# Performance work log

Measured on AMD Instinct MI355X. Metric: run time of the kernel, lower is better.

The kernel has to match this reference:

```python
import jax, jax.numpy as jnp
import numpy as np

IN_C, OUT_C, MAX_SIZE = 512, 256, 256
N = MAX_SIZE * MAX_SIZE  # 65536 nodes
E = MAX_SIZE * MAX_SIZE  # 65536 edges (before self loops)
NEG_SLOPE = 0.2


def setup_inputs() -> dict:
    key = jax.random.key(0)
    ks = jax.random.split(key, 12)
    s = 1.0 / np.sqrt(IN_C)
    so = 1.0 / np.sqrt(OUT_C)
    return {
        "x": jax.random.normal(ks[0], (N, IN_C), dtype=jnp.float32),
        "x_mask": jnp.ones((N,), dtype=bool),
        "edge_index": jax.random.randint(ks[1], (2, E), 0, N),
        "edge_mask": jnp.ones((E,), dtype=bool),
        "vaild_mask": jnp.ones((MAX_SIZE, MAX_SIZE), dtype=bool),
        # self-loop Linear
        "W_self": jax.random.uniform(ks[2], (IN_C, OUT_C), jnp.float32, -s, s),
        "b_self": jax.random.uniform(ks[3], (OUT_C,), jnp.float32, -s, s),
        # GATv2Conv params (heads=1)
        "W_l": jax.random.uniform(ks[4], (IN_C, OUT_C), jnp.float32, -s, s),
        "b_l": jnp.zeros((OUT_C,), jnp.float32),
        "W_r": jax.random.uniform(ks[5], (IN_C, OUT_C), jnp.float32, -s, s),
        "b_r": jnp.zeros((OUT_C,), jnp.float32),
        "att": jax.random.uniform(ks[6], (OUT_C,), jnp.float32, -so, so),
        "conv_bias": jnp.zeros((OUT_C,), jnp.float32),
        # sk classifier (out_channels -> 1)
        "W_cls": jax.random.uniform(ks[7], (OUT_C, 1), jnp.float32, -so, so),
        "b_cls": jax.random.uniform(ks[8], (1,), jnp.float32, -so, so),
    }


def _forward(x, edge_index, W_self, b_self, W_l, b_l, W_r, b_r, att,
             conv_bias, W_cls, b_cls):
    n = x.shape[0]
    # PyG GATv2Conv adds self-loops by default
    loops = jnp.arange(n, dtype=edge_index.dtype)
    src = jnp.concatenate([edge_index[0], loops])
    dst = jnp.concatenate([edge_index[1], loops])

    x_l = x @ W_l + b_l  # source-side transform (n, out)
    x_r = x @ W_r + b_r  # target-side transform (n, out)

    # per-edge GATv2 attention logits
    h = jax.nn.leaky_relu(x_l[src] + x_r[dst], NEG_SLOPE)  # (Etot, out)
    e = h @ att  # (Etot,)

    # segment softmax over incoming edges of each target node
    m = jnp.full((n,), -jnp.inf, dtype=e.dtype).at[dst].max(e)
    p = jnp.exp(e - m[dst])
    denom = jax.ops.segment_sum(p, dst, num_segments=n)
    alpha = p / denom[dst]

    x_neigh = jax.ops.segment_sum(alpha[:, None] * x_l[src], dst,
                                  num_segments=n) + conv_bias
    x_out = (x @ W_self + b_self) + x_neigh

    # sinkhorn-style row softmax channel (sk_channel=1, n1=n2=max_size)
    ms = MAX_SIZE
    sk = (x_out @ W_cls + b_cls).reshape(ms, ms)
    sk = jax.nn.softmax(sk, axis=-1)
    x_out = x_out + sk.reshape(-1, 1)
    # n1*n2 == max_size**2, so the padded output equals x_out
    return x_out


def reference(x, x_mask, edge_index, edge_mask, vaild_mask, W_self, b_self,
              W_l, b_l, W_r, b_r, att, conv_bias, W_cls, b_cls):
    # masks are all-True (fully valid case): x_valid = x, edges all kept
    return _forward(x, edge_index, W_self, b_self, W_l, b_l, W_r, b_r, att,
                    conv_bias, W_cls, b_cls)
```

## Files before the change

kernel.cpp:

```cpp
#include <hip/hip_runtime.h>
#include <hip/hip_bf16.h>
#include <stdint.h>

#define NNODE 65536
#define NEDGE 65536
#define ETOT  (NNODE + NEDGE)
#define INC   512
#define OUTC  256
#define NEG_SLOPE 0.2f
#define SLOTCAP 32

typedef __attribute__((ext_vector_type(8))) __bf16 bf16x8;
typedef __attribute__((ext_vector_type(4))) float f32x4;

__device__ __forceinline__ float b2f(unsigned short u) {
  return __uint_as_float(((unsigned int)u) << 16);
}
__device__ __forceinline__ unsigned short f2b(float f) {
  unsigned int u = __float_as_uint(f);
  u += 0x7fffu + ((u >> 16) & 1u);
  return (unsigned short)(u >> 16);
}
__device__ __forceinline__ unsigned int pk2(float lo, float hi) {
  return (unsigned int)f2b(lo) | ((unsigned int)f2b(hi) << 16);
}
__device__ __forceinline__ float lrelu(float v) {
  return v > 0.f ? v : NEG_SLOPE * v;
}

__global__ __launch_bounds__(256) void cvt_x_kernel(const float* __restrict__ x,
                                                    unsigned short* __restrict__ xb) {
  size_t i = ((size_t)blockIdx.x * 256 + threadIdx.x) * 4;
  float4 v = *(const float4*)(x + i);
  ushort4 o = { f2b(v.x), f2b(v.y), f2b(v.z), f2b(v.w) };
  *(ushort4*)(xb + i) = o;
}

__global__ __launch_bounds__(256) void prep_w_kernel(
    const float* __restrict__ Wl, const float* __restrict__ Wr, const float* __restrict__ Ws,
    const float* __restrict__ bl, const float* __restrict__ br, const float* __restrict__ bs,
    unsigned short* __restrict__ WT, float* __restrict__ bcat) {
  int i = blockIdx.x * 256 + threadIdx.x;
  if (i < 768 * 512) {
    int o = i >> 9, k = i & 511;
    float v;
    if (o < 256)      v = Wl[k * 256 + o];
    else if (o < 512) v = Wr[k * 256 + (o - 256)];
    else              v = Ws[k * 256 + (o - 512)];
    WT[i] = f2b(v);
  }
  if (i < 768) {
    bcat[i] = (i < 256) ? bl[i] : (i < 512 ? br[i - 256] : bs[i - 512]);
  }
}

__global__ __launch_bounds__(256) void gemm_kernel(
    const unsigned short* __restrict__ Xb,
    const unsigned short* __restrict__ WT,
    const float* __restrict__ bcat,
    unsigned short* __restrict__ xl,
    unsigned short* __restrict__ xr,
    float* __restrict__ outSelf) {
  __shared__ __align__(16) char smem[49152];
  unsigned short* sm = (unsigned short*)smem;

  const int wid = blockIdx.x;
  const int xcd = wid & 7;
  const int local = wid >> 3;
  const int by = local % 6;
  const int rowt = xcd * 64 + local / 6;
  const int rowBase = rowt * 128;
  const int colBase = by * 128;

  const int tid = threadIdx.x;
  const int lane = tid & 63;
  const int w = tid >> 6;
  const int wm = (w >> 1) * 64;
  const int wn = (w & 1) * 64;

  f32x4 acc[4][4] = {};

  auto stage = [&](int kk, int buf) {
#pragma unroll
    for (int c = 0; c < 2; ++c) {
      const int qb = w * 64 + c * 256;
      const int q = qb + lane;
      const int sl = (q & 3) ^ ((q >> 3) & 3);
      const unsigned short* gA = Xb + (size_t)(rowBase + (q >> 2)) * 512 + kk + sl * 8;
      __builtin_amdgcn_global_load_lds(
          (const __attribute__((address_space(1))) void*)gA,
          (__attribute__((address_space(3))) void*)(sm + buf * 8192 + qb * 8), 16, 0, 0);
      const unsigned short* gB = WT + (size_t)(colBase + (q >> 2)) * 512 + kk + sl * 8;
      __builtin_amdgcn_global_load_lds(
          (const __attribute__((address_space(1))) void*)gB,
          (__attribute__((address_space(3))) void*)(sm + buf * 8192 + 4096 + qb * 8), 16, 0, 0);
    }
  };

#define COMPUTE(bufidx) { \
    const unsigned short* As = sm + (bufidx) * 8192; \
    const unsigned short* Bs = As + 4096; \
    bf16x8 a_frag[4], b_frag[4]; \
    _Pragma("unroll") \
    for (int m = 0; m < 4; ++m) { \
      const int rA = wm + m * 16 + (lane & 15); \
      a_frag[m] = *(const bf16x8*)&As[rA * 32 + (((lane >> 4) ^ ((rA >> 1) & 3)) << 3)]; \
    } \
    _Pragma("unroll") \
    for (int n = 0; n < 4; ++n) { \
      const int rB = wn + n * 16 + (lane & 15); \
      b_frag[n] = *(const bf16x8*)&Bs[rB * 32 + (((lane >> 4) ^ ((rB >> 1) & 3)) << 3)]; \
    } \
    __builtin_amdgcn_s_setprio(1); \
    _Pragma("unroll") \
    for (int m = 0; m < 4; ++m) \
      _Pragma("unroll") \
      for (int n = 0; n < 4; ++n) \
        acc[m][n] = __builtin_amdgcn_mfma_f32_16x16x32_bf16(a_frag[m], b_frag[n], acc[m][n], 0, 0, 0); \
    __builtin_amdgcn_s_setprio(0); \
  }

  stage(0, 0);
  stage(32, 1);

  for (int t = 0; t < 14; ++t) {
    const int buf = t % 3;
    stage((t + 2) * 32, (t + 2) % 3);
    asm volatile("s_waitcnt vmcnt(8)" ::: "memory");
    __builtin_amdgcn_s_barrier();
    __builtin_amdgcn_sched_barrier(0);
    COMPUTE(buf);
    __builtin_amdgcn_sched_barrier(0);
    __builtin_amdgcn_s_barrier();
  }
  asm volatile("s_waitcnt vmcnt(4)" ::: "memory");
  __builtin_amdgcn_s_barrier();
  __builtin_amdgcn_sched_barrier(0);
  COMPUTE(2);
  __builtin_amdgcn_sched_barrier(0);
  __builtin_amdgcn_s_barrier();
  asm volatile("s_waitcnt vmcnt(0)" ::: "memory");
  __builtin_amdgcn_s_barrier();
  __builtin_amdgcn_sched_barrier(0);
  COMPUTE(0);
#undef COMPUTE

  const int colOff = (by & 1) * 128;
  if (by < 4) {
    unsigned short* dst = (by < 2) ? xl : xr;
    float* eps = (float*)smem + w * 1088;
    float biasn[4];
#pragma unroll
    for (int n = 0; n < 4; ++n) biasn[n] = bcat[colBase + wn + n * 16 + (lane & 15)];
#pragma unroll
    for (int m = 0; m < 4; ++m) {
      __syncthreads();
#pragma unroll
      for (int n = 0; n < 4; ++n)
#pragma unroll
        for (int j = 0; j < 4; ++j)
          eps[((lane >> 4) * 4 + j) * 68 + n * 16 + (lane & 15)] = acc[m][n][j] + biasn[n];
      __syncthreads();
#pragma unroll
      for (int it = 0; it < 2; ++it) {
        const int r16 = (lane >> 3) + it * 8;
        const int c8 = (lane & 7) * 8;
        const float* src = eps + r16 * 68 + c8;
        float4 v0 = *(const float4*)src;
        float4 v1 = *(const float4*)(src + 4);
        uint4 o;
        o.x = pk2(v0.x, v0.y);
        o.y = pk2(v0.z, v0.w);
        o.z = pk2(v1.x, v1.y);
        o.w = pk2(v1.z, v1.w);
        const int grow = rowBase + wm + m * 16 + r16;
        const int gcol = colOff + wn + c8;
        *(uint4*)(dst + (size_t)grow * 256 + gcol) = o;
      }
    }
  } else {
#pragma unroll
    for (int n = 0; n < 4; ++n) {
      const int col = colBase + wn + n * 16 + (lane & 15);
      const float bias = bcat[col];
#pragma unroll
      for (int m = 0; m < 4; ++m) {
#pragma unroll
        for (int j = 0; j < 4; ++j) {
          const int row = rowBase + wm + m * 16 + (lane >> 4) * 4 + j;
          outSelf[(size_t)row * 256 + (col - 512)] = acc[m][n][j] + bias;
        }
      }
    }
  }
}

__global__ __launch_bounds__(256) void edge_logit_kernel(
    const int* __restrict__ ei,
    const unsigned short* __restrict__ xl,
    const unsigned short* __restrict__ xr,
    const float* __restrict__ att,
    int* __restrict__ cnt,
    int* __restrict__ slot_src,
    float* __restrict__ slot_e) {
  const int j = blockIdx.x * 8 + (threadIdx.x >> 5);
  const int lane = threadIdx.x & 31;
  int src, dst;
  if (j < NEDGE) { src = ei[j]; dst = ei[NEDGE + j]; }
  else           { src = j - NEDGE; dst = src; }
  const int c = lane * 8;
  uint4 ul = *(const uint4*)(xl + (size_t)src * 256 + c);
  uint4 ur = *(const uint4*)(xr + (size_t)dst * 256 + c);
  float4 a0 = *(const float4*)(att + c);
  float4 a1 = *(const float4*)(att + c + 4);
  float s = lrelu(b2f((unsigned short)ul.x) + b2f((unsigned short)ur.x)) * a0.x
          + lrelu(b2f((unsigned short)(ul.x >> 16)) + b2f((unsigned short)(ur.x >> 16))) * a0.y
          + lrelu(b2f((unsigned short)ul.y) + b2f((unsigned short)ur.y)) * a0.z
          + lrelu(b2f((unsigned short)(ul.y >> 16)) + b2f((unsigned short)(ur.y >> 16))) * a0.w
          + lrelu(b2f((unsigned short)ul.z) + b2f((unsigned short)ur.z)) * a1.x
          + lrelu(b2f((unsigned short)(ul.z >> 16)) + b2f((unsigned short)(ur.z >> 16))) * a1.y
          + lrelu(b2f((unsigned short)ul.w) + b2f((unsigned short)ur.w)) * a1.z
          + lrelu(b2f((unsigned short)(ul.w >> 16)) + b2f((unsigned short)(ur.w >> 16))) * a1.w;
#pragma unroll
  for (int off = 16; off; off >>= 1) s += __shfl_xor(s, off);
  if (lane == 0) {
    const int pos = atomicAdd(&cnt[dst], 1);
    if (pos < SLOTCAP) {
      slot_src[dst * SLOTCAP + pos] = src;
      slot_e[dst * SLOTCAP + pos] = s;
    }
  }
}

__global__ __launch_bounds__(256) void node_kernel(
    const int* __restrict__ cnt,
    const int* __restrict__ slot_src, const float* __restrict__ slot_e,
    const unsigned short* __restrict__ xl,
    const float* __restrict__ conv_bias,
    float* __restrict__ out,
    const float* __restrict__ Wcls, const float* __restrict__ bcls,
    float* __restrict__ logits) {
  const int n = blockIdx.x * 4 + (threadIdx.x >> 6);
  const int lane = threadIdx.x & 63;
  const int base = n * SLOTCAP;
  const int deg = cnt[n];

  float m = -1e30f;
  for (int k = 0; k < deg; ++k) m = fmaxf(m, slot_e[base + k]);
  float denom = 0.f;
  for (int k = 0; k < deg; ++k) denom += __expf(slot_e[base + k] - m);
  const float inv = 1.f / denom;

  const int c = lane * 4;
  float4 accv = {0.f, 0.f, 0.f, 0.f};
  for (int k = 0; k < deg; ++k) {
    const float alpha = __expf(slot_e[base + k] - m) * inv;
    const int src = slot_src[base + k];
    ushort4 u = *(const ushort4*)(xl + (size_t)src * 256 + c);
    accv.x += alpha * b2f(u.x);
    accv.y += alpha * b2f(u.y);
    accv.z += alpha * b2f(u.z);
    accv.w += alpha * b2f(u.w);
  }
  const size_t o = (size_t)n * 256 + c;
  float4 cur = *(const float4*)(out + o);
  float4 cb = *(const float4*)(conv_bias + c);
  cur.x += accv.x + cb.x;
  cur.y += accv.y + cb.y;
  cur.z += accv.z + cb.z;
  cur.w += accv.w + cb.w;
  *(float4*)(out + o) = cur;

  float4 wc = *(const float4*)(Wcls + c);
  float part = cur.x * wc.x + cur.y * wc.y + cur.z * wc.z + cur.w * wc.w;
#pragma unroll
  for (int off = 32; off; off >>= 1) part += __shfl_xor(part, off, 64);
  if (lane == 0) logits[n] = part + bcls[0];
}

__global__ __launch_bounds__(256) void sk_kernel(const float* __restrict__ logits,
                                                 float* __restrict__ out) {
  __shared__ float sv[256];
  __shared__ float red[256];
  const int r = blockIdx.x >> 2;
  const int q = blockIdx.x & 3;
  const int t = threadIdx.x;
  const float v = logits[r * 256 + t];
  red[t] = v;
  __syncthreads();
  for (int d = 128; d; d >>= 1) {
    if (t < d) red[t] = fmaxf(red[t], red[t + d]);
    __syncthreads();
  }
  const float mx = red[0];
  __syncthreads();
  const float p = __expf(v - mx);
  red[t] = p;
  __syncthreads();
  for (int d = 128; d; d >>= 1) {
    if (t < d) red[t] += red[t + d];
    __syncthreads();
  }
  const float sum = red[0];
  sv[t] = p / sum;
  __syncthreads();
  const size_t rowbase = (size_t)r * 256 * 256;
  for (int i = q * 64; i < q * 64 + 64; ++i) {
    out[rowbase + (size_t)i * 256 + t] += sv[i];
  }
}

extern "C" void kernel_launch(void* const* d_in, const int* in_sizes, int n_in,
                              void* d_out, int out_size, void* d_ws, size_t ws_size,
                              hipStream_t stream) {
  const float* x        = (const float*)d_in[0];
  const int*   ei       = (const int*)d_in[2];
  const float* W_self   = (const float*)d_in[5];
  const float* b_self   = (const float*)d_in[6];
  const float* W_l      = (const float*)d_in[7];
  const float* b_l      = (const float*)d_in[8];
  const float* W_r      = (const float*)d_in[9];
  const float* b_r      = (const float*)d_in[10];
  const float* att      = (const float*)d_in[11];
  const float* conv_bias= (const float*)d_in[12];
  const float* W_cls    = (const float*)d_in[13];
  const float* b_cls    = (const float*)d_in[14];
  float* out = (float*)d_out;

  char* ws = (char*)d_ws;
  size_t off = 0;
  auto alloc = [&](size_t bytes) {
    char* p = ws + off;
    off += (bytes + 255) & ~(size_t)255;
    return p;
  };
  unsigned short* xb   = (unsigned short*)alloc((size_t)NNODE * INC * 2);
  unsigned short* WT   = (unsigned short*)alloc((size_t)768 * 512 * 2);
  float*          bcat = (float*)alloc(768 * 4);
  unsigned short* xlb  = (unsigned short*)alloc((size_t)NNODE * OUTC * 2);
  unsigned short* xrb  = (unsigned short*)alloc((size_t)NNODE * OUTC * 2);
  int*            cnt  = (int*)alloc((size_t)NNODE * 4);
  float*          logits  = (float*)alloc((size_t)NNODE * 4);
  int*   slot_src = (int*)xb;
  float* slot_e   = (float*)(xb + (size_t)NNODE * SLOTCAP * 2);
  (void)ws_size; (void)in_sizes; (void)n_in; (void)out_size;

  hipMemsetAsync(cnt, 0, (size_t)NNODE * 4, stream);

  cvt_x_kernel<<<(NNODE * INC) / (256 * 4), 256, 0, stream>>>(x, xb);
  prep_w_kernel<<<(768 * 512 + 255) / 256, 256, 0, stream>>>(W_l, W_r, W_self, b_l, b_r, b_self, WT, bcat);
  gemm_kernel<<<3072, 256, 0, stream>>>(xb, WT, bcat, xlb, xrb, out);
  edge_logit_kernel<<<ETOT / 8, 256, 0, stream>>>(ei, xlb, xrb, att, cnt, slot_src, slot_e);
  node_kernel<<<NNODE / 4, 256, 0, stream>>>(cnt, slot_src, slot_e, xlb, conv_bias,
                                             out, W_cls, b_cls, logits);
  sk_kernel<<<1024, 256, 0, stream>>>(logits, out);
}
```

Baseline: 202.1 us.

## Enlarge GEMM tiles to 256x256 with 512 threads and store self term as bf16

The GEMM moves from 128x128 tiles with 256 threads to 256x256 tiles with 8 waves and BK=64. Operand reuse per LDS load goes up, and the pipeline changes from a triple buffer to a double buffer using 128KB of LDS. The self-loop projection is now written as a bf16 buffer instead of fp32 straight into out, and the node kernel reads it back and adds it. This cuts GEMM store traffic and drops a read-modify-write of out, at the cost of precision on the self term, lower occupancy, and fewer blocks (768) to spread across CUs.

Measured after the change: 205.4 us. About the same (+1.6%).

```diff
diff --git a/kernel.cpp b/kernel.cpp
--- a/kernel.cpp
+++ b/kernel.cpp
@@ -54,142 +54,123 @@
   }
 }
 
-__global__ __launch_bounds__(256) void gemm_kernel(
+__global__ __launch_bounds__(512) void gemm_kernel(
     const unsigned short* __restrict__ Xb,
     const unsigned short* __restrict__ WT,
     const float* __restrict__ bcat,
     unsigned short* __restrict__ xl,
     unsigned short* __restrict__ xr,
-    float* __restrict__ outSelf) {
-  __shared__ __align__(16) char smem[49152];
+    unsigned short* __restrict__ xs) {
+  __shared__ __align__(16) char smem[131072];
   unsigned short* sm = (unsigned short*)smem;
 
   const int wid = blockIdx.x;
   const int xcd = wid & 7;
   const int local = wid >> 3;
-  const int by = local % 6;
-  const int rowt = xcd * 64 + local / 6;
-  const int rowBase = rowt * 128;
-  const int colBase = by * 128;
+  const int by = local % 3;
+  const int rowt = xcd * 32 + local / 3;
+  const int rowBase = rowt * 256;
+  const int colBase = by * 256;
 
   const int tid = threadIdx.x;
   const int lane = tid & 63;
   const int w = tid >> 6;
-  const int wm = (w >> 1) * 64;
-  const int wn = (w & 1) * 64;
-
-  f32x4 acc[4][4] = {};
+  const int wm = (w >> 2) * 128;
+  const int wn = (w & 3) * 64;
+
+  f32x4 acc[8][4] = {};
 
   auto stage = [&](int kk, int buf) {
-#pragma unroll
-    for (int c = 0; c < 2; ++c) {
-      const int qb = w * 64 + c * 256;
-      const int q = qb + lane;
-      const int sl = (q & 3) ^ ((q >> 3) & 3);
-      const unsigned short* gA = Xb + (size_t)(rowBase + (q >> 2)) * 512 + kk + sl * 8;
+    const int q = tid;
+    const int slot_sw = q & 7;
+#pragma unroll
+    for (int l = 0; l < 4; ++l) {
+      const int r = l * 64 + (q >> 3);
+      const int slot = slot_sw ^ (r & 7);
+      const unsigned short* gA = Xb + (size_t)(rowBase + r) * 512 + kk + slot * 8;
       __builtin_amdgcn_global_load_lds(
           (const __attribute__((address_space(1))) void*)gA,
-          (__attribute__((address_space(3))) void*)(sm + buf * 8192 + qb * 8), 16, 0, 0);
-      const unsigned short* gB = WT + (size_t)(colBase + (q >> 2)) * 512 + kk + sl * 8;
+          (__attribute__((address_space(3))) void*)(sm + buf * 32768 + l * 4096 + q * 8), 16, 0, 0);
+      const unsigned short* gB = WT + (size_t)(colBase + r) * 512 + kk + slot * 8;
       __builtin_amdgcn_global_load_lds(
           (const __attribute__((address_space(1))) void*)gB,
-          (__attribute__((address_space(3))) void*)(sm + buf * 8192 + 4096 + qb * 8), 16, 0, 0);
+          (__attribute__((address_space(3))) void*)(sm + buf * 32768 + 16384 + l * 4096 + q * 8), 16, 0, 0);
     }
   };
 
 #define COMPUTE(bufidx) { \
-    const unsigned short* As = sm + (bufidx) * 8192; \
-    const unsigned short* Bs = As + 4096; \
-    bf16x8 a_frag[4], b_frag[4]; \
+    const unsigned short* As = sm + (bufidx) * 32768; \
+    const unsigned short* Bs = As + 16384; \
     _Pragma("unroll") \
-    for (int m = 0; m < 4; ++m) { \
-      const int rA = wm + m * 16 + (lane & 15); \
-      a_frag[m] = *(const bf16x8*)&As[rA * 32 + (((lane >> 4) ^ ((rA >> 1) & 3)) << 3)]; \
+    for (int kh = 0; kh < 2; ++kh) { \
+      bf16x8 bfr[4]; \
+      _Pragma("unroll") \
+      for (int n = 0; n < 4; ++n) { \
+        const int rB = wn + n * 16 + (lane & 15); \
+        const int sB = (kh * 4 + (lane >> 4)) ^ (rB & 7); \
+        bfr[n] = *(const bf16x8*)&Bs[rB * 64 + sB * 8]; \
+      } \
+      _Pragma("unroll") \
+      for (int m = 0; m < 8; ++m) { \
+        const int rA = wm + m * 16 + (lane & 15); \
+        const int sA = (kh * 4 + (lane >> 4)) ^ (rA & 7); \
+        bf16x8 afr = *(const bf16x8*)&As[rA * 64 + sA * 8]; \
+        __builtin_amdgcn_s_setprio(1); \
+        _Pragma("unroll") \
+        for (int n = 0; n < 4; ++n) \
+          acc[m][n] = __builtin_amdgcn_mfma_f32_16x16x32_bf16(afr, bfr[n], acc[m][n], 0, 0, 0); \
+        __builtin_amdgcn_s_setprio(0); \
+      } \
     } \
-    _Pragma("unroll") \
-    for (int n = 0; n < 4; ++n) { \
-      const int rB = wn + n * 16 + (lane & 15); \
-      b_frag[n] = *(const bf16x8*)&Bs[rB * 32 + (((lane >> 4) ^ ((rB >> 1) & 3)) << 3)]; \
-    } \
-    __builtin_amdgcn_s_setprio(1); \
-    _Pragma("unroll") \
-    for (int m = 0; m < 4; ++m) \
-      _Pragma("unroll") \
-      for (int n = 0; n < 4; ++n) \
-        acc[m][n] = __builtin_amdgcn_mfma_f32_16x16x32_bf16(a_frag[m], b_frag[n], acc[m][n], 0, 0, 0); \
-    __builtin_amdgcn_s_setprio(0); \
   }
 
   stage(0, 0);
-  stage(32, 1);
-
-  for (int t = 0; t < 14; ++t) {
-    const int buf = t % 3;
-    stage((t + 2) * 32, (t + 2) % 3);
-    asm volatile("s_waitcnt vmcnt(8)" ::: "memory");
-    __builtin_amdgcn_s_barrier();
+  stage(64, 1);
+  asm volatile("s_waitcnt vmcnt(8)" ::: "memory");
+  __builtin_amdgcn_s_barrier();
+
+  for (int t = 0; t < 8; ++t) {
+    const int buf = t & 1;
     __builtin_amdgcn_sched_barrier(0);
     COMPUTE(buf);
     __builtin_amdgcn_sched_barrier(0);
     __builtin_amdgcn_s_barrier();
-  }
-  asm volatile("s_waitcnt vmcnt(4)" ::: "memory");
-  __builtin_amdgcn_s_barrier();
-  __builtin_amdgcn_sched_barrier(0);
-  COMPUTE(2);
-  __builtin_amdgcn_sched_barrier(0);
-  __builtin_amdgcn_s_barrier();
-  asm volatile("s_waitcnt vmcnt(0)" ::: "memory");
-  __builtin_amdgcn_s_barrier();
-  __builtin_amdgcn_sched_barrier(0);
-  COMPUTE(0);
+    if (t + 2 < 8) {
+      stage((t + 2) * 64, buf);
+      asm volatile("s_waitcnt vmcnt(8)" ::: "memory");
+    } else {
+      asm volatile("s_waitcnt vmcnt(0)" ::: "memory");
+    }
+    __builtin_amdgcn_s_barrier();
+  }
 #undef COMPUTE
 
-  const int colOff = (by & 1) * 128;
-  if (by < 4) {
-    unsigned short* dst = (by < 2) ? xl : xr;
+  {
+    unsigned short* dst = (by == 0) ? xl : (by == 1) ? xr : xs;
     float* eps = (float*)smem + w * 1088;
     float biasn[4];
 #pragma unroll
     for (int n = 0; n < 4; ++n) biasn[n] = bcat[colBase + wn + n * 16 + (lane & 15)];
 #pragma unroll
-    for (int m = 0; m < 4; ++m) {
-      __syncthreads();
+    for (int m = 0; m < 8; ++m) {
 #pragma unroll
       for (int n = 0; n < 4; ++n)
 #pragma unroll
         for (int j = 0; j < 4; ++j)
           eps[((lane >> 4) * 4 + j) * 68 + n * 16 + (lane & 15)] = acc[m][n][j] + biasn[n];
-      __syncthreads();
 #pragma unroll
       for (int it = 0; it < 2; ++it) {
-        const int r16 = (lane >> 3) + it * 8;
+        const int r16 = it * 8 + (lane >> 3);
         const int c8 = (lane & 7) * 8;
-        const float* src = eps + r16 * 68 + c8;
-        float4 v0 = *(const float4*)src;
-        float4 v1 = *(const float4*)(src + 4);
+        const float* srcp = eps + r16 * 68 + c8;
+        float4 v0 = *(const float4*)srcp;
+        float4 v1 = *(const float4*)(srcp + 4);
         uint4 o;
         o.x = pk2(v0.x, v0.y);
         o.y = pk2(v0.z, v0.w);
         o.z = pk2(v1.x, v1.y);
         o.w = pk2(v1.z, v1.w);
-        const int grow = rowBase + wm + m * 16 + r16;
-        const int gcol = colOff + wn + c8;
-        *(uint4*)(dst + (size_t)grow * 256 + gcol) = o;
-      }
-    }
-  } else {
-#pragma unroll
-    for (int n = 0; n < 4; ++n) {
-      const int col = colBase + wn + n * 16 + (lane & 15);
-      const float bias = bcat[col];
-#pragma unroll
-      for (int m = 0; m < 4; ++m) {
-#pragma unroll
-        for (int j = 0; j < 4; ++j) {
-          const int row = rowBase + wm + m * 16 + (lane >> 4) * 4 + j;
-          outSelf[(size_t)row * 256 + (col - 512)] = acc[m][n][j] + bias;
-        }
+        *(uint4*)(dst + (size_t)(rowBase + wm + m * 16 + r16) * 256 + wn + c8) = o;
       }
     }
   }
@@ -236,6 +217,7 @@
     const int* __restrict__ cnt,
     const int* __restrict__ slot_src, const float* __restrict__ slot_e,
     const unsigned short* __restrict__ xl,
+    const unsigned short* __restrict__ xs,
     const float* __restrict__ conv_bias,
     float* __restrict__ out,
     const float* __restrict__ Wcls, const float* __restrict__ bcls,
@@ -262,13 +244,14 @@
     accv.z += alpha * b2f(u.z);
     accv.w += alpha * b2f(u.w);
   }
+  ushort4 s4 = *(const ushort4*)(xs + (size_t)n * 256 + c);
+  float4 cb = *(const float4*)(conv_bias + c);
+  float4 cur;
+  cur.x = b2f(s4.x) + accv.x + cb.x;
+  cur.y = b2f(s4.y) + accv.y + cb.y;
+  cur.z = b2f(s4.z) + accv.z + cb.z;
+  cur.w = b2f(s4.w) + accv.w + cb.w;
   const size_t o = (size_t)n * 256 + c;
-  float4 cur = *(const float4*)(out + o);
-  float4 cb = *(const float4*)(conv_bias + c);
-  cur.x += accv.x + cb.x;
-  cur.y += accv.y + cb.y;
-  cur.z += accv.z + cb.z;
-  cur.w += accv.w + cb.w;
   *(float4*)(out + o) = cur;
 
   float4 wc = *(const float4*)(Wcls + c);
@@ -339,6 +322,7 @@
   float*          bcat = (float*)alloc(768 * 4);
   unsigned short* xlb  = (unsigned short*)alloc((size_t)NNODE * OUTC * 2);
   unsigned short* xrb  = (unsigned short*)alloc((size_t)NNODE * OUTC * 2);
+  unsigned short* xsb  = (unsigned short*)alloc((size_t)NNODE * OUTC * 2);
   int*            cnt  = (int*)alloc((size_t)NNODE * 4);
   float*          logits  = (float*)alloc((size_t)NNODE * 4);
   int*   slot_src = (int*)xb;
@@ -349,9 +333,9 @@
 
   cvt_x_kernel<<<(NNODE * INC) / (256 * 4), 256, 0, stream>>>(x, xb);
   prep_w_kernel<<<(768 * 512 + 255) / 256, 256, 0, stream>>>(W_l, W_r, W_self, b_l, b_r, b_self, WT, bcat);
-  gemm_kernel<<<3072, 256, 0, stream>>>(xb, WT, bcat, xlb, xrb, out);
+  gemm_kernel<<<768, 512, 0, stream>>>(xb, WT, bcat, xlb, xrb, xsb);
   edge_logit_kernel<<<ETOT / 8, 256, 0, stream>>>(ei, xlb, xrb, att, cnt, slot_src, slot_e);
-  node_kernel<<<NNODE / 4, 256, 0, stream>>>(cnt, slot_src, slot_e, xlb, conv_bias,
+  node_kernel<<<NNODE / 4, 256, 0, stream>>>(cnt, slot_src, slot_e, xlb, xsb, conv_bias,
                                              out, W_cls, b_cls, logits);
   sk_kernel<<<1024, 256, 0, stream>>>(logits, out);
 }
```
